# Optimization experiments

Measured on AMD Instinct MI355X. Metric: run time of the kernel, lower is better.

Reference implementation:

```python
import jax, jax.numpy as jnp
import numpy as np

EPS = 1e-7

def _cell(x_t, h, s_l, s_B, lambda_log, B):
    # x_t: [b, d], h/s_l: [b, n], s_B: [b, n, d], lambda_log: [n], B: [n, d]
    lam = jnp.exp(-jnp.exp(lambda_log))                    # [n]
    gamma = jnp.sqrt(1.0 - lam * lam + EPS)                # [n]
    Bx = x_t @ B.T                                         # [b, n]
    h1 = lam * h + gamma * Bx
    dlam = -lam * jnp.exp(lambda_log)                      # d lambda / d lambda_log
    s_l1 = h * dlam + lam * s_l + Bx * (-lam / gamma) * dlam
    s_B1 = lam[None, :, None] * s_B + gamma[None, :, None] * x_t[:, None, :]
    return h1, s_l1, s_B1

def setup_inputs() -> dict:
    key = jax.random.key(0)
    k1, k2, k3, k4 = jax.random.split(key, 4)
    S, BT, D, N, O = 256, 32, 128, 128, 128
    x = jax.random.normal(k1, (S, BT, D), dtype=jnp.float32)
    # torch init: lambda_log = log(-0.5*log(u1)) with rmin=0, rmax=1
    u1 = jax.random.uniform(k2, (N,), dtype=jnp.float32, minval=0.01, maxval=0.99)
    lambda_log = jnp.log(-0.5 * jnp.log(u1))
    B = jax.random.normal(k3, (N, D), dtype=jnp.float32) / np.sqrt(D)
    C = jax.random.normal(k4, (O, N), dtype=jnp.float32) / np.sqrt(N)
    return {"x": x, "lambda_log": lambda_log, "B": B, "C": C}

def reference(x, lambda_log, B, C):
    S, BT, D = x.shape
    N = B.shape[0]
    h0 = jnp.zeros((BT, N), x.dtype)
    sl0 = jnp.zeros((BT, N), x.dtype)
    sB0 = jnp.zeros((BT, N, D), x.dtype)

    def scan_fn(carry, x_t):
        h, s_l, s_B = carry
        h1, s_l1, s_B1 = _cell(x_t, h, s_l, s_B, lambda_log, B)
        return (h1, s_l1, s_B1), h1

    (hT, _, _), hs = jax.lax.scan(scan_fn, (h0, sl0, sB0), x)
    outputs = jnp.einsum('sbn,on->sbo', hs, C)  # h_t @ C^T per step
    return outputs, hT
```

## Files before the change

### kernel.cpp

```cpp
#include <hip/hip_runtime.h>

#define S_DIM 256
#define BT_DIM 32
#define D_DIM 128
#define N_DIM 128
#define O_DIM 128
#define SB (S_DIM * BT_DIM)
#define EPS 1e-7f

typedef short s16x8 __attribute__((ext_vector_type(8)));
typedef float fx4   __attribute__((ext_vector_type(4)));

__device__ __forceinline__ unsigned pk_bf16(float a, float b) {
    unsigned r;
    asm("v_cvt_pk_bf16_f32 %0, %1, %2" : "=v"(r) : "v"(a), "v"(b));
    return r;
}
__device__ __forceinline__ s16x8 cvt8hi(const float4 f0, const float4 f1) {
    union { unsigned u[4]; s16x8 v; } r;
    r.u[0] = pk_bf16(f0.x, f0.y);
    r.u[1] = pk_bf16(f0.z, f0.w);
    r.u[2] = pk_bf16(f1.x, f1.y);
    r.u[3] = pk_bf16(f1.z, f1.w);
    return r.v;
}

__global__ __launch_bounds__(256) void k1_gemm_scan(const float* __restrict__ X,
                                                    const float* __restrict__ lamlog,
                                                    const float* __restrict__ Bm,
                                                    const float* __restrict__ Cm,
                                                    unsigned short* __restrict__ hs_hi,
                                                    unsigned short* __restrict__ Chi,
                                                    float* __restrict__ hT) {
    const int t = threadIdx.x;

    if (blockIdx.x >= 256) {
        const int id = (blockIdx.x - 256) * 256 + t;
        const float4 f0 = reinterpret_cast<const float4*>(Cm)[id * 2];
        const float4 f1 = reinterpret_cast<const float4*>(Cm)[id * 2 + 1];
        *reinterpret_cast<uint4*>(Chi + (size_t)id * 8) =
            make_uint4(pk_bf16(f0.x, f0.y), pk_bf16(f0.z, f0.w),
                       pk_bf16(f1.x, f1.y), pk_bf16(f1.z, f1.w));
        return;
    }

    __shared__ unsigned short Bhi[16][136];
    __shared__ float Bxs[S_DIM][17];
    __shared__ float carr[16][17];

    const int d  = blockIdx.x;
    const int b  = (d & 7) * 4 + (d >> 6);
    const int n0 = ((d >> 3) & 7) * 16;

    #pragma unroll
    for (int q = 0; q < 2; ++q) {
        const int id4 = t + 256 * q;
        const int row = id4 >> 5, c4 = id4 & 31;
        const float4 f = *reinterpret_cast<const float4*>(Bm + (size_t)(n0 + row) * D_DIM + c4 * 4);
        *reinterpret_cast<uint2*>(&Bhi[row][c4 * 4]) =
            make_uint2(pk_bf16(f.x, f.y), pk_bf16(f.z, f.w));
    }
    __syncthreads();

    const int w  = t >> 6, l = t & 63;
    const int lr = l & 15;
    const int lk = (l >> 4) * 8;

    {
        s16x8 bh[4];
        #pragma unroll
        for (int sl = 0; sl < 4; ++sl)
            bh[sl] = *reinterpret_cast<const s16x8*>(&Bhi[lr][sl * 32 + lk]);

        const float* __restrict__ xb = X + (size_t)b * D_DIM;
        #pragma unroll
        for (int q = 0; q < 4; ++q) {
            const int s0 = (w * 4 + q) * 16;
            const float* __restrict__ xr = xb + (size_t)(s0 + lr) * (BT_DIM * D_DIM);
            s16x8 ah[4];
            #pragma unroll
            for (int sl = 0; sl < 4; ++sl) {
                const float4 f0 = *reinterpret_cast<const float4*>(xr + sl * 32 + lk);
                const float4 f1 = *reinterpret_cast<const float4*>(xr + sl * 32 + lk + 4);
                ah[sl] = cvt8hi(f0, f1);
            }
            fx4 acc = {0.f, 0.f, 0.f, 0.f};
            #pragma unroll
            for (int sl = 0; sl < 4; ++sl)
                acc = __builtin_amdgcn_mfma_f32_16x16x32_bf16(ah[sl], bh[sl], acc, 0, 0, 0);
            #pragma unroll
            for (int r = 0; r < 4; ++r)
                Bxs[s0 + (l >> 4) * 4 + r][lr] = acc[r];
        }
    }
    __syncthreads();

    const int j = t & 15;
    const int c = t >> 4;
    const float ll    = lamlog[n0 + j];
    const float lam   = expf(-expf(ll));
    const float gamma = sqrtf(1.f - lam * lam + EPS);
    const float l2 = lam * lam, l4 = l2 * l2, l8 = l4 * l4;
    const float lam16 = l8 * l8;

    float h = 0.f;
    #pragma unroll
    for (int i = 0; i < 16; ++i)
        h = fmaf(lam, h, gamma * Bxs[c * 16 + i][j]);
    carr[c][j] = h;
    __syncthreads();

    float carrv[16];
    #pragma unroll
    for (int cp = 0; cp < 16; ++cp) carrv[cp] = carr[cp][j];
    float Hb = 0.f;
    #pragma unroll
    for (int cp = 0; cp < 16; ++cp)
        if (cp < c) Hb = fmaf(lam16, Hb, carrv[cp]);

    h = Hb;
    #pragma unroll
    for (int i = 0; i < 16; ++i) {
        h = fmaf(lam, h, gamma * Bxs[c * 16 + i][j]);
        const size_t rg = (size_t)(c * 16 + i) * BT_DIM + b;
        hs_hi[rg * N_DIM + n0 + j] = (unsigned short)pk_bf16(h, h);
    }
    if (c == 15) hT[b * N_DIM + n0 + j] = h;
}

__global__ __launch_bounds__(256) void k2_outgemm(const unsigned short* __restrict__ hs_hi,
                                                  const unsigned short* __restrict__ Chi,
                                                  float* __restrict__ out) {
    __shared__ unsigned short Hs[32][136];

    const int t  = threadIdx.x;
    const int r0 = blockIdx.x * 32;

    {
        const int row = t >> 3, ch = t & 7;
        const unsigned short* src = hs_hi + (size_t)(r0 + row) * N_DIM + ch * 16;
        *reinterpret_cast<uint4*>(&Hs[row][ch * 16])     = *reinterpret_cast<const uint4*>(src);
        *reinterpret_cast<uint4*>(&Hs[row][ch * 16 + 8]) = *reinterpret_cast<const uint4*>(src + 8);
    }
    __syncthreads();

    const int w  = t >> 6, l = t & 63;
    const int lr = l & 15;
    const int lk = (l >> 4) * 8;
    const int rt = w & 1;

    s16x8 ah[4];
    #pragma unroll
    for (int sl = 0; sl < 4; ++sl)
        ah[sl] = *reinterpret_cast<const s16x8*>(&Hs[16 * rt + lr][sl * 32 + lk]);

    #pragma unroll
    for (int q = 0; q < 4; ++q) {
        const int o0 = (w >> 1) * 64 + q * 16;
        fx4 acc = {0.f, 0.f, 0.f, 0.f};
        #pragma unroll
        for (int sl = 0; sl < 4; ++sl) {
            const s16x8 bh = *reinterpret_cast<const s16x8*>(&Chi[(size_t)(o0 + lr) * N_DIM + sl * 32 + lk]);
            acc = __builtin_amdgcn_mfma_f32_16x16x32_bf16(ah[sl], bh, acc, 0, 0, 0);
        }
        const int rw = r0 + 16 * rt + (l >> 4) * 4;
        #pragma unroll
        for (int r = 0; r < 4; ++r)
            out[(size_t)(rw + r) * O_DIM + o0 + lr] = acc[r];
    }
}

extern "C" void kernel_launch(void* const* d_in, const int* in_sizes, int n_in,
                              void* d_out, int out_size, void* d_ws, size_t ws_size,
                              hipStream_t stream) {
    const float* x          = (const float*)d_in[0];
    const float* lambda_log = (const float*)d_in[1];
    const float* B          = (const float*)d_in[2];
    const float* C          = (const float*)d_in[3];

    float* out = (float*)d_out;
    float* hT  = out + (size_t)SB * O_DIM;

    unsigned short* hs_hi = (unsigned short*)d_ws;
    unsigned short* Chi   = hs_hi + (size_t)SB * N_DIM;

    k1_gemm_scan<<<264, 256, 0, stream>>>(x, lambda_log, B, C, hs_hi, Chi, hT);
    k2_outgemm<<<256, 256, 0, stream>>>(hs_hi, Chi, out);
}
```

Baseline: 69.73 us.

## Fuse scan and output GEMM into one kernel with per-batch atomic barrier

Merges the Bx GEMM plus scan kernel and the output projection kernel into a single launch of 256 blocks. Blocks sharing a batch index wait on a global atomic counter, then each computes a slice of the output GEMM by reading hs back from global memory. C is converted to bf16 in registers by every block instead of in a separate pass. This removes one kernel launch and the Chi buffer, but adds a memset, a spin-wait inter-block barrier that assumes all blocks are co-resident, and redundant C loads.

```diff
diff --git a/kernel.cpp b/kernel.cpp
--- a/kernel.cpp
+++ b/kernel.cpp
@@ -25,32 +25,23 @@
     return r.v;
 }
 
-__global__ __launch_bounds__(256) void k1_gemm_scan(const float* __restrict__ X,
+__global__ __launch_bounds__(256, 1) void fused_lru(const float* __restrict__ X,
                                                     const float* __restrict__ lamlog,
                                                     const float* __restrict__ Bm,
                                                     const float* __restrict__ Cm,
+                                                    unsigned* __restrict__ cnt,
                                                     unsigned short* __restrict__ hs_hi,
-                                                    unsigned short* __restrict__ Chi,
+                                                    float* __restrict__ out,
                                                     float* __restrict__ hT) {
-    const int t = threadIdx.x;
-
-    if (blockIdx.x >= 256) {
-        const int id = (blockIdx.x - 256) * 256 + t;
-        const float4 f0 = reinterpret_cast<const float4*>(Cm)[id * 2];
-        const float4 f1 = reinterpret_cast<const float4*>(Cm)[id * 2 + 1];
-        *reinterpret_cast<uint4*>(Chi + (size_t)id * 8) =
-            make_uint4(pk_bf16(f0.x, f0.y), pk_bf16(f0.z, f0.w),
-                       pk_bf16(f1.x, f1.y), pk_bf16(f1.z, f1.w));
-        return;
-    }
-
     __shared__ unsigned short Bhi[16][136];
     __shared__ float Bxs[S_DIM][17];
     __shared__ float carr[16][17];
 
+    const int t = threadIdx.x;
     const int d  = blockIdx.x;
     const int b  = (d & 7) * 4 + (d >> 6);
-    const int n0 = ((d >> 3) & 7) * 16;
+    const int nt = (d >> 3) & 7;
+    const int n0 = nt * 16;
 
     #pragma unroll
     for (int q = 0; q < 2; ++q) {
@@ -93,80 +84,87 @@
                 Bxs[s0 + (l >> 4) * 4 + r][lr] = acc[r];
         }
     }
-    __syncthreads();
 
-    const int j = t & 15;
-    const int c = t >> 4;
-    const float ll    = lamlog[n0 + j];
-    const float lam   = expf(-expf(ll));
-    const float gamma = sqrtf(1.f - lam * lam + EPS);
-    const float l2 = lam * lam, l4 = l2 * l2, l8 = l4 * l4;
-    const float lam16 = l8 * l8;
-
-    float h = 0.f;
+    s16x8 ch[4][4];
     #pragma unroll
-    for (int i = 0; i < 16; ++i)
-        h = fmaf(lam, h, gamma * Bxs[c * 16 + i][j]);
-    carr[c][j] = h;
-    __syncthreads();
-
-    float carrv[16];
-    #pragma unroll
-    for (int cp = 0; cp < 16; ++cp) carrv[cp] = carr[cp][j];
-    float Hb = 0.f;
-    #pragma unroll
-    for (int cp = 0; cp < 16; ++cp)
-        if (cp < c) Hb = fmaf(lam16, Hb, carrv[cp]);
-
-    h = Hb;
-    #pragma unroll
-    for (int i = 0; i < 16; ++i) {
-        h = fmaf(lam, h, gamma * Bxs[c * 16 + i][j]);
-        const size_t rg = (size_t)(c * 16 + i) * BT_DIM + b;
-        hs_hi[rg * N_DIM + n0 + j] = (unsigned short)pk_bf16(h, h);
-    }
-    if (c == 15) hT[b * N_DIM + n0 + j] = h;
-}
-
-__global__ __launch_bounds__(256) void k2_outgemm(const unsigned short* __restrict__ hs_hi,
-                                                  const unsigned short* __restrict__ Chi,
-                                                  float* __restrict__ out) {
-    __shared__ unsigned short Hs[32][136];
-
-    const int t  = threadIdx.x;
-    const int r0 = blockIdx.x * 32;
-
-    {
-        const int row = t >> 3, ch = t & 7;
-        const unsigned short* src = hs_hi + (size_t)(r0 + row) * N_DIM + ch * 16;
-        *reinterpret_cast<uint4*>(&Hs[row][ch * 16])     = *reinterpret_cast<const uint4*>(src);
-        *reinterpret_cast<uint4*>(&Hs[row][ch * 16 + 8]) = *reinterpret_cast<const uint4*>(src + 8);
+    for (int q = 0; q < 4; ++q) {
+        const int o0 = (w >> 1) * 64 + q * 16;
+        const float* __restrict__ cr = Cm + (size_t)(o0 + lr) * N_DIM;
+        #pragma unroll
+        for (int sl = 0; sl < 4; ++sl) {
+            const float4 f0 = *reinterpret_cast<const float4*>(cr + sl * 32 + lk);
+            const float4 f1 = *reinterpret_cast<const float4*>(cr + sl * 32 + lk + 4);
+            ch[q][sl] = cvt8hi(f0, f1);
+        }
     }
     __syncthreads();
 
-    const int w  = t >> 6, l = t & 63;
-    const int lr = l & 15;
-    const int lk = (l >> 4) * 8;
-    const int rt = w & 1;
+    {
+        const int j = t & 15;
+        const int c = t >> 4;
+        const float ll    = lamlog[n0 + j];
+        const float lam   = expf(-expf(ll));
+        const float gamma = sqrtf(1.f - lam * lam + EPS);
+        const float l2 = lam * lam, l4 = l2 * l2, l8 = l4 * l4;
+        const float lam16 = l8 * l8;
 
+        float h = 0.f;
+        #pragma unroll
+        for (int i = 0; i < 16; ++i)
+            h = fmaf(lam, h, gamma * Bxs[c * 16 + i][j]);
+        carr[c][j] = h;
+        __syncthreads();
+
+        float carrv[16];
+        #pragma unroll
+        for (int cp = 0; cp < 16; ++cp) carrv[cp] = carr[cp][j];
+        float Hb = 0.f;
+        #pragma unroll
+        for (int cp = 0; cp < 16; ++cp)
+            if (cp < c) Hb = fmaf(lam16, Hb, carrv[cp]);
+
+        h = Hb;
+        #pragma unroll
+        for (int i = 0; i < 16; ++i) {
+            h = fmaf(lam, h, gamma * Bxs[c * 16 + i][j]);
+            const size_t rg = (size_t)(c * 16 + i) * BT_DIM + b;
+            hs_hi[rg * N_DIM + n0 + j] = (unsigned short)pk_bf16(h, h);
+        }
+        if (c == 15) hT[b * N_DIM + n0 + j] = h;
+    }
+
+    __syncthreads();
+    __threadfence();
+    __syncthreads();
+    if (t == 0) {
+        atomicAdd(&cnt[b], 1u);
+        while (__hip_atomic_load(&cnt[b], __ATOMIC_RELAXED, __HIP_MEMORY_SCOPE_AGENT) < 8u)
+            __builtin_amdgcn_s_sleep(8);
+    }
+    __syncthreads();
+    __threadfence();
+
+    const int st  = w & 1;
+    const int s0c = nt * 32 + st * 16;
+
+    const unsigned short* __restrict__ hr =
+        hs_hi + ((size_t)(s0c + lr) * BT_DIM + b) * N_DIM;
     s16x8 ah[4];
     #pragma unroll
     for (int sl = 0; sl < 4; ++sl)
-        ah[sl] = *reinterpret_cast<const s16x8*>(&Hs[16 * rt + lr][sl * 32 + lk]);
+        ah[sl] = *reinterpret_cast<const s16x8*>(&hr[sl * 32 + lk]);
 
     #pragma unroll
     for (int q = 0; q < 4; ++q) {
         const int o0 = (w >> 1) * 64 + q * 16;
         fx4 acc = {0.f, 0.f, 0.f, 0.f};
         #pragma unroll
-        for (int sl = 0; sl < 4; ++sl) {
-            const s16x8 bh = *reinterpret_cast<const s16x8*>(&Chi[(size_t)(o0 + lr) * N_DIM + sl * 32 + lk]);
-            acc = __builtin_amdgcn_mfma_f32_16x16x32_bf16(ah[sl], bh, acc, 0, 0, 0);
-        }
-        const int rw = r0 + 16 * rt + (l >> 4) * 4;
+        for (int sl = 0; sl < 4; ++sl)
+            acc = __builtin_amdgcn_mfma_f32_16x16x32_bf16(ah[sl], ch[q][sl], acc, 0, 0, 0);
+        const int sw = s0c + (l >> 4) * 4;
         #pragma unroll
         for (int r = 0; r < 4; ++r)
-            out[(size_t)(rw + r) * O_DIM + o0 + lr] = acc[r];
+            out[((size_t)(sw + r) * BT_DIM + b) * O_DIM + o0 + lr] = acc[r];
     }
 }
 
@@ -181,9 +179,9 @@
     float* out = (float*)d_out;
     float* hT  = out + (size_t)SB * O_DIM;
 
-    unsigned short* hs_hi = (unsigned short*)d_ws;
-    unsigned short* Chi   = hs_hi + (size_t)SB * N_DIM;
+    unsigned* cnt = (unsigned*)d_ws;
+    unsigned short* hs_hi = (unsigned short*)((char*)d_ws + 256);
 
-    k1_gemm_scan<<<264, 256, 0, stream>>>(x, lambda_log, B, C, hs_hi, Chi, hT);
-    k2_outgemm<<<256, 256, 0, stream>>>(hs_hi, Chi, out);
+    hipMemsetAsync(cnt, 0, 128, stream);
+    fused_lru<<<256, 256, 0, stream>>>(x, lambda_log, B, C, cnt, hs_hi, out, hT);
 }
```

New measurement: 114.8 us. 64.7% more time.
